# Optimization experiments

Measured on AMD Instinct MI355X. Metric: run time of the kernel, lower is better.

Reference implementation:

```python
import jax, jax.numpy as jnp
import numpy as np

EPS = 1e-9
ROUTING_ITERATIONS = 3


def setup_inputs() -> dict:
    key = jax.random.key(0)
    k1, k2 = jax.random.split(key)
    B, Nin, Din = 32, 2048, 16   # batch, input capsules, input capsule dim
    Nout, Dout = 64, 32          # output capsules, output capsule dim
    x = jax.random.normal(k1, (B, Nin, Din), dtype=jnp.float32)
    # transformation weights W[i, j, d, k] (shared across batch)
    W = jax.random.normal(k2, (Nin, Nout, Dout, Din), dtype=jnp.float32) * 0.05
    bias = jnp.zeros((Nout, Dout), dtype=jnp.float32)
    return {"x": x, "W": W, "bias": bias}


def _squash(s):
    # squash along last axis (capsule vector dim)
    sq_norm = jnp.sum(jnp.square(s), axis=-1, keepdims=True)
    scale = sq_norm / (1.0 + sq_norm)
    return scale * s / jnp.sqrt(sq_norm + EPS)


def reference(x, W, bias):
    # u_hat[b,i,j,d] = sum_k W[i,j,d,k] * x[b,i,k]
    u_hat = jnp.einsum('ijdk,bik->bijd', W, x)
    B, Nin, Nout, Dout = u_hat.shape
    b_log = jnp.zeros((B, Nin, Nout), dtype=u_hat.dtype)  # routing logits
    v = None
    for it in range(ROUTING_ITERATIONS):
        c = jax.nn.softmax(b_log, axis=2)                 # coupling coeffs over Nout
        s = jnp.einsum('bij,bijd->bjd', c, u_hat) + bias  # [B, Nout, Dout]
        v = _squash(s)
        if it < ROUTING_ITERATIONS - 1:
            b_log = b_log + jnp.einsum('bijd,bjd->bij', u_hat, v)
    return v  # [B, Nout, Dout]
```

## Files before the change

kernel.cpp:

```cpp
#include <hip/hip_runtime.h>
#include <hip/hip_bf16.h>
#include <stdint.h>


#define CB    32
#define NIN   2048
#define DIN   16
#define NOUT  64
#define DOUT  32
#define IPB   8
#define NCB   (NIN / IPB)
#define WI    (NOUT * DOUT * DIN)
#define WELEM ((size_t)NIN * WI)

typedef __attribute__((ext_vector_type(8)))  short bf16x8;
typedef __attribute__((ext_vector_type(16))) float f32x16;
typedef _Float16 h2 __attribute__((ext_vector_type(2)));

#define VOFF 0
#define COFF 135168
#define XOFF_IT 143616
#define SMEM_IT  153856
#define SMEM_P0  10240

static __device__ __forceinline__ uint32_t pack_bf2(float a, float b) {
    __hip_bfloat162 hh = __float22bfloat162_rn(make_float2(a, b));
    uint32_t u; __builtin_memcpy(&u, &hh, 4); return u;
}
static __device__ __forceinline__ uint16_t f2bf(float v) {
    return (uint16_t)(pack_bf2(v, 0.f) & 0xffffu);
}
static __device__ __forceinline__ float bf2f(uint16_t u) {
    uint32_t v = (uint32_t)u << 16; float f; __builtin_memcpy(&f, &v, 4); return f;
}
static __device__ __forceinline__ uint32_t pack_h2(float a, float b) {
    h2 r; r.x = (_Float16)a; r.y = (_Float16)b;
    uint32_t u; __builtin_memcpy(&u, &r, 4); return u;
}
static __device__ __forceinline__ h2 as_h2(uint32_t u) {
    h2 r; __builtin_memcpy(&r, &u, 4); return r;
}

__global__ __launch_bounds__(1024, 4) void caps_pass0(
    const float* __restrict__ x, const float* __restrict__ Wf,
    uint32_t* __restrict__ WhOut, uint16_t* __restrict__ s_partial)
{
    extern __shared__ char smem[];
    uint32_t* x_lds = (uint32_t*)smem;

    const int cb = blockIdx.x;
    const int t  = threadIdx.x;
    const int w  = t >> 6, l = t & 63;
    const int bl = l & 31, h = l >> 5;
    const int j0 = w * 4;

    {
        const int b = t >> 5, i = (t >> 2) & 7, k4 = (t & 3) * 4;
        const float4 xv = *(const float4*)(x + ((size_t)b * NIN + cb * IPB + i) * DIN + k4);
        x_lds[(i * 32 + b) * 10 + (k4 >> 1)]     = pack_bf2(xv.x, xv.y);
        x_lds[(i * 32 + b) * 10 + (k4 >> 1) + 1] = pack_bf2(xv.z, xv.w);
    }
    __syncthreads();

    f32x16 sacc[4];
#pragma unroll
    for (int jj = 0; jj < 4; ++jj) sacc[jj] = (f32x16)0.0f;

#pragma unroll 1
    for (int i = 0; i < IPB; ++i) {
        const size_t wbase = (size_t)(cb * IPB + i) * WI;
        bf16x8 bfr;
        {
            uint32_t uu[4];
            const uint32_t* xp = &x_lds[(i * 32 + bl) * 10 + h * 4];
            uu[0] = xp[0]; uu[1] = xp[1]; uu[2] = xp[2]; uu[3] = xp[3];
            __builtin_memcpy(&bfr, uu, 16);
        }
#pragma unroll
        for (int jj = 0; jj < 4; ++jj) {
            const int j = j0 + jj;
            const size_t eoff = wbase + (size_t)(j * 32 + bl) * 16 + h * 8;
            const float4* wp = (const float4*)(Wf + eoff);
            const float4 a4 = wp[0], b4 = wp[1];
            uint32_t uu[4];
            uu[0] = pack_bf2(a4.x, a4.y); uu[1] = pack_bf2(a4.z, a4.w);
            uu[2] = pack_bf2(b4.x, b4.y); uu[3] = pack_bf2(b4.z, b4.w);
            bf16x8 afr; __builtin_memcpy(&afr, uu, 16);
            uint4 st; st.x = uu[0]; st.y = uu[1]; st.z = uu[2]; st.w = uu[3];
            *(uint4*)(WhOut + (eoff >> 1)) = st;
            sacc[jj] = __builtin_amdgcn_mfma_f32_32x32x16_bf16(afr, bfr, sacc[jj], 0, 0, 0);
        }
    }

#pragma unroll
    for (int jj = 0; jj < 4; ++jj) {
        const int j = j0 + jj;
#pragma unroll
        for (int r = 0; r < 16; ++r) {
            const int d = (r & 3) + 8 * (r >> 2) + 4 * h;
            s_partial[(size_t)cb * (2048 * 32) + (size_t)(j * 32 + d) * 32 + bl] =
                f2bf(sacc[jj][r] * (1.0f / 64.0f));
        }
    }
}

template <int IT>
__global__ __launch_bounds__(1024, 4) void caps_it(
    const float* __restrict__ x, const uint16_t* __restrict__ Wh,
    const float* __restrict__ v_prev, const float* __restrict__ blog_in,
    float* __restrict__ blog_out, uint16_t* __restrict__ s_partial)
{
    extern __shared__ char smem[];
    uint32_t* v_lds = (uint32_t*)(smem + VOFF);
    float*    c_lds = (float*)(smem + COFF);
    uint32_t* x_lds = (uint32_t*)(smem + XOFF_IT);

    const int cb = blockIdx.x;
    const int t  = threadIdx.x;
    const int w  = t >> 6, l = t & 63;
    const int bl = l & 31, h = l >> 5;
    const int j0 = w * 4;

    {
        const int b = t >> 5, i = (t >> 2) & 7, k4 = (t & 3) * 4;
        const float4 xv = *(const float4*)(x + ((size_t)b * NIN + cb * IPB + i) * DIN + k4);
        x_lds[(i * 32 + b) * 10 + (k4 >> 1)]     = pack_bf2(xv.x, xv.y);
        x_lds[(i * 32 + b) * 10 + (k4 >> 1) + 1] = pack_bf2(xv.z, xv.w);
    }
#pragma unroll 4
    for (int rep = 0; rep < 32; ++rep) {
        const int idx = rep * 1024 + t;
        const int b = idx >> 10, j = (idx >> 4) & 63, dp = idx & 15;
        const float2 vv = *(const float2*)(v_prev + ((size_t)b * NOUT + j) * DOUT + dp * 2);
        v_lds[(j * 16 + dp) * 33 + b] = pack_h2(vv.x, vv.y);
    }
    __syncthreads();

    f32x16 sacc[4];
#pragma unroll
    for (int jj = 0; jj < 4; ++jj) sacc[jj] = (f32x16)0.0f;

    constexpr int base_dp[8] = {0, 1, 4, 5, 8, 9, 12, 13};

#pragma unroll 1
    for (int i = 0; i < IPB; ++i) {
        const int ig = cb * IPB + i;
        const size_t wbase = (size_t)ig * WI;

        bf16x8 bfr;
        {
            uint32_t uu[4];
            const uint32_t* xp = &x_lds[(i * 32 + bl) * 10 + h * 4];
            uu[0] = xp[0]; uu[1] = xp[1]; uu[2] = xp[2]; uu[3] = xp[3];
            __builtin_memcpy(&bfr, uu, 16);
        }

        uint32_t Dp[4][8];
#pragma unroll
        for (int jj = 0; jj < 4; ++jj) {
            const int j = j0 + jj;
            const bf16x8 afr = *(const bf16x8*)(Wh + wbase + (size_t)(j * 32 + bl) * 16 + h * 8);
            const f32x16 D = __builtin_amdgcn_mfma_f32_32x32x16_bf16(afr, bfr, (f32x16)0.0f, 0, 0, 0);
            float acc = 0.f;
#pragma unroll
            for (int rp = 0; rp < 8; ++rp) {
                const int dp = base_dp[rp] + 2 * h;
                const uint32_t pk = pack_h2(D[2 * rp], D[2 * rp + 1]);
                Dp[jj][rp] = pk;
                acc = __builtin_amdgcn_fdot2(as_h2(pk), as_h2(v_lds[(j * 16 + dp) * 33 + bl]), acc, false);
            }
            acc += __shfl_xor(acc, 32);
            if (h == 0) c_lds[j * 33 + bl] = acc;
        }
        __syncthreads();

#pragma unroll
        for (int rr = 0; rr < 2; ++rr) {
            const int b = w * 2 + rr;
            float bv = c_lds[l * 33 + b];
            if (IT == 2) bv += blog_in[((size_t)b * NIN + ig) * NOUT + l];
            if (IT == 1) blog_out[((size_t)b * NIN + ig) * NOUT + l] = bv;
            float m = bv;
#pragma unroll
            for (int o = 32; o; o >>= 1) m = fmaxf(m, __shfl_xor(m, o));
            const float e = __expf(bv - m);
            float s = e;
#pragma unroll
            for (int o = 32; o; o >>= 1) s += __shfl_xor(s, o);
            c_lds[l * 33 + b] = e / s;
        }
        __syncthreads();

#pragma unroll
        for (int jj = 0; jj < 4; ++jj) {
            const int j = j0 + jj;
            const float cv = c_lds[j * 33 + bl];
#pragma unroll
            for (int rp = 0; rp < 8; ++rp) {
                const h2 hv = as_h2(Dp[jj][rp]);
                sacc[jj][2 * rp]     += cv * (float)hv.x;
                sacc[jj][2 * rp + 1] += cv * (float)hv.y;
            }
        }
        __syncthreads();
    }

#pragma unroll
    for (int jj = 0; jj < 4; ++jj) {
        const int j = j0 + jj;
#pragma unroll
        for (int r = 0; r < 16; ++r) {
            const int d = (r & 3) + 8 * (r >> 2) + 4 * h;
            s_partial[(size_t)cb * (2048 * 32) + (size_t)(j * 32 + d) * 32 + bl] =
                f2bf(sacc[jj][r]);
        }
    }
}

__global__ __launch_bounds__(256) void caps_squash(
    const uint16_t* __restrict__ sp, const float* __restrict__ bias,
    float* __restrict__ vout)
{
    const int j  = blockIdx.x >> 2;
    const int bq = blockIdx.x & 3;
    const int t  = threadIdx.x;
    const int d  = t >> 3;
    const int blq = t & 7;
    const int b  = bq * 8 + blq;

    const uint16_t* p = sp + (size_t)(j * 32 + d) * 32 + b;
    float s0 = 0.f, s1 = 0.f, s2 = 0.f, s3 = 0.f;
#pragma unroll 4
    for (int c = 0; c < NCB; c += 4) {
        s0 += bf2f(p[(size_t)(c + 0) * (2048 * 32)]);
        s1 += bf2f(p[(size_t)(c + 1) * (2048 * 32)]);
        s2 += bf2f(p[(size_t)(c + 2) * (2048 * 32)]);
        s3 += bf2f(p[(size_t)(c + 3) * (2048 * 32)]);
    }
    const float sv = ((s0 + s1) + (s2 + s3)) + bias[j * DOUT + d];

    float sq = sv * sv;
    sq += __shfl_xor(sq, 8);
    sq += __shfl_xor(sq, 16);
    sq += __shfl_xor(sq, 32);

    __shared__ float sh[4][8];
    if ((t & 63) < 8) sh[t >> 6][t & 7] = sq;
    __syncthreads();
    const float tot = sh[0][blq] + sh[1][blq] + sh[2][blq] + sh[3][blq];
    const float scale = (tot / (1.0f + tot)) * rsqrtf(tot + 1e-9f);
    vout[(size_t)b * (NOUT * DOUT) + j * DOUT + d] = scale * sv;
}

extern "C" void kernel_launch(void* const* d_in, const int* in_sizes, int n_in,
                              void* d_out, int out_size, void* d_ws, size_t ws_size,
                              hipStream_t stream) {
    const float* x    = (const float*)d_in[0];
    const float* W    = (const float*)d_in[1];
    const float* bias = (const float*)d_in[2];
    float* out = (float*)d_out;

    char* base = (char*)d_ws;
    uint32_t* Wh    = (uint32_t*)base;
    float*    blog  = (float*)(base + WELEM * 2);
    uint16_t* spart = (uint16_t*)(base + WELEM * 2 + (size_t)CB * NIN * NOUT * 4);
    float*    vbuf  = (float*)(base + WELEM * 2 + (size_t)CB * NIN * NOUT * 4
                               + (size_t)NCB * 2048 * 32 * 2);
    (void)ws_size;

    hipFuncSetAttribute(reinterpret_cast<const void*>(caps_pass0),
                        hipFuncAttributeMaxDynamicSharedMemorySize, SMEM_P0);
    hipFuncSetAttribute(reinterpret_cast<const void*>(caps_it<1>),
                        hipFuncAttributeMaxDynamicSharedMemorySize, SMEM_IT);
    hipFuncSetAttribute(reinterpret_cast<const void*>(caps_it<2>),
                        hipFuncAttributeMaxDynamicSharedMemorySize, SMEM_IT);

    caps_pass0<<<NCB, 1024, SMEM_P0, stream>>>(x, W, (uint32_t*)Wh, spart);
    caps_squash<<<NOUT * 4, 256, 0, stream>>>(spart, bias, vbuf);

    caps_it<1><<<NCB, 1024, SMEM_IT, stream>>>(x, (const uint16_t*)Wh, vbuf, nullptr, blog, spart);
    caps_squash<<<NOUT * 4, 256, 0, stream>>>(spart, bias, vbuf);

    caps_it<2><<<NCB, 1024, SMEM_IT, stream>>>(x, (const uint16_t*)Wh, vbuf, blog, nullptr, spart);
    caps_squash<<<NOUT * 4, 256, 0, stream>>>(spart, bias, out);
}
```

Measured before the change: 273.3 us.

## Fuse all routing passes into one cooperative kernel with grid syncs

```diff
diff --git a/kernel.cpp b/kernel.cpp
--- a/kernel.cpp
+++ b/kernel.cpp
@@ -1,6 +1,9 @@
 #include <hip/hip_runtime.h>
+#include <hip/hip_cooperative_groups.h>
 #include <hip/hip_bf16.h>
 #include <stdint.h>
+
+namespace cg = cooperative_groups;
 
 
 #define CB    32
@@ -17,11 +20,11 @@
 typedef __attribute__((ext_vector_type(16))) float f32x16;
 typedef _Float16 h2 __attribute__((ext_vector_type(2)));
 
-#define VOFF 0
-#define COFF 135168
-#define XOFF_IT 143616
-#define SMEM_IT  153856
-#define SMEM_P0  10240
+#define VOFF    0
+#define COFF    135168
+#define CSTRIDE 2112
+#define XOFF    152064
+#define SMEM_FUSED 162304
 
 static __device__ __forceinline__ uint32_t pack_bf2(float a, float b) {
     __hip_bfloat162 hh = __float22bfloat162_rn(make_float2(a, b));
@@ -41,26 +44,33 @@
     h2 r; __builtin_memcpy(&r, &u, 4); return r;
 }
 
-__global__ __launch_bounds__(1024, 4) void caps_pass0(
-    const float* __restrict__ x, const float* __restrict__ Wf,
-    uint32_t* __restrict__ WhOut, uint16_t* __restrict__ s_partial)
-{
-    extern __shared__ char smem[];
-    uint32_t* x_lds = (uint32_t*)smem;
-
-    const int cb = blockIdx.x;
-    const int t  = threadIdx.x;
-    const int w  = t >> 6, l = t & 63;
+
+static __device__ __forceinline__ void stage_x(const float* __restrict__ x,
+                                               uint32_t* x_lds, int cb, int t) {
+    const int b = t >> 5, i = (t >> 2) & 7, k4 = (t & 3) * 4;
+    const float4 xv = *(const float4*)(x + ((size_t)b * NIN + cb * IPB + i) * DIN + k4);
+    x_lds[(i * 32 + b) * 10 + (k4 >> 1)]     = pack_bf2(xv.x, xv.y);
+    x_lds[(i * 32 + b) * 10 + (k4 >> 1) + 1] = pack_bf2(xv.z, xv.w);
+}
+
+static __device__ __forceinline__ void stage_v(const float* __restrict__ v_prev,
+                                               uint32_t* v_lds, int t) {
+#pragma unroll 4
+    for (int rep = 0; rep < 32; ++rep) {
+        const int idx = rep * 1024 + t;
+        const int b = idx >> 10, j = (idx >> 4) & 63, dp = idx & 15;
+        const float2 vv = *(const float2*)(v_prev + ((size_t)b * NOUT + j) * DOUT + dp * 2);
+        v_lds[(j * 16 + dp) * 33 + b] = pack_h2(vv.x, vv.y);
+    }
+}
+
+static __device__ __forceinline__ void pass0_body(
+    const float* __restrict__ Wf, uint32_t* __restrict__ WhOut,
+    uint16_t* __restrict__ s_partial, const uint32_t* x_lds, int cb, int t)
+{
+    const int w = t >> 6, l = t & 63;
     const int bl = l & 31, h = l >> 5;
     const int j0 = w * 4;
-
-    {
-        const int b = t >> 5, i = (t >> 2) & 7, k4 = (t & 3) * 4;
-        const float4 xv = *(const float4*)(x + ((size_t)b * NIN + cb * IPB + i) * DIN + k4);
-        x_lds[(i * 32 + b) * 10 + (k4 >> 1)]     = pack_bf2(xv.x, xv.y);
-        x_lds[(i * 32 + b) * 10 + (k4 >> 1) + 1] = pack_bf2(xv.z, xv.w);
-    }
-    __syncthreads();
 
     f32x16 sacc[4];
 #pragma unroll
@@ -105,37 +115,15 @@
 }
 
 template <int IT>
-__global__ __launch_bounds__(1024, 4) void caps_it(
-    const float* __restrict__ x, const uint16_t* __restrict__ Wh,
-    const float* __restrict__ v_prev, const float* __restrict__ blog_in,
-    float* __restrict__ blog_out, uint16_t* __restrict__ s_partial)
-{
-    extern __shared__ char smem[];
-    uint32_t* v_lds = (uint32_t*)(smem + VOFF);
-    float*    c_lds = (float*)(smem + COFF);
-    uint32_t* x_lds = (uint32_t*)(smem + XOFF_IT);
-
-    const int cb = blockIdx.x;
-    const int t  = threadIdx.x;
-    const int w  = t >> 6, l = t & 63;
+static __device__ __forceinline__ void it_body(
+    const uint16_t* __restrict__ Wh, const float* __restrict__ blog_in,
+    float* __restrict__ blog_out, uint16_t* __restrict__ s_partial,
+    const uint32_t* v_lds, float* c_lds, const uint32_t* x_lds, int cb, int t)
+{
+    const int w = t >> 6, l = t & 63;
     const int bl = l & 31, h = l >> 5;
     const int j0 = w * 4;
 
-    {
-        const int b = t >> 5, i = (t >> 2) & 7, k4 = (t & 3) * 4;
-        const float4 xv = *(const float4*)(x + ((size_t)b * NIN + cb * IPB + i) * DIN + k4);
-        x_lds[(i * 32 + b) * 10 + (k4 >> 1)]     = pack_bf2(xv.x, xv.y);
-        x_lds[(i * 32 + b) * 10 + (k4 >> 1) + 1] = pack_bf2(xv.z, xv.w);
-    }
-#pragma unroll 4
-    for (int rep = 0; rep < 32; ++rep) {
-        const int idx = rep * 1024 + t;
-        const int b = idx >> 10, j = (idx >> 4) & 63, dp = idx & 15;
-        const float2 vv = *(const float2*)(v_prev + ((size_t)b * NOUT + j) * DOUT + dp * 2);
-        v_lds[(j * 16 + dp) * 33 + b] = pack_h2(vv.x, vv.y);
-    }
-    __syncthreads();
-
     f32x16 sacc[4];
 #pragma unroll
     for (int jj = 0; jj < 4; ++jj) sacc[jj] = (f32x16)0.0f;
@@ -144,6 +132,7 @@
 
 #pragma unroll 1
     for (int i = 0; i < IPB; ++i) {
+        float* cp = c_lds + (i & 1) * CSTRIDE;
         const int ig = cb * IPB + i;
         const size_t wbase = (size_t)ig * WI;
 
@@ -155,7 +144,6 @@
             __builtin_memcpy(&bfr, uu, 16);
         }
 
-        uint32_t Dp[4][8];
 #pragma unroll
         for (int jj = 0; jj < 4; ++jj) {
             const int j = j0 + jj;
@@ -165,19 +153,18 @@
 #pragma unroll
             for (int rp = 0; rp < 8; ++rp) {
                 const int dp = base_dp[rp] + 2 * h;
-                const uint32_t pk = pack_h2(D[2 * rp], D[2 * rp + 1]);
-                Dp[jj][rp] = pk;
-                acc = __builtin_amdgcn_fdot2(as_h2(pk), as_h2(v_lds[(j * 16 + dp) * 33 + bl]), acc, false);
+                h2 dpk; dpk.x = (_Float16)D[2 * rp]; dpk.y = (_Float16)D[2 * rp + 1];
+                acc = __builtin_amdgcn_fdot2(dpk, as_h2(v_lds[(j * 16 + dp) * 33 + bl]), acc, false);
             }
             acc += __shfl_xor(acc, 32);
-            if (h == 0) c_lds[j * 33 + bl] = acc;
+            if (h == 0) cp[j * 33 + bl] = acc;
         }
         __syncthreads();
 
 #pragma unroll
         for (int rr = 0; rr < 2; ++rr) {
             const int b = w * 2 + rr;
-            float bv = c_lds[l * 33 + b];
+            float bv = cp[l * 33 + b];
             if (IT == 2) bv += blog_in[((size_t)b * NIN + ig) * NOUT + l];
             if (IT == 1) blog_out[((size_t)b * NIN + ig) * NOUT + l] = bv;
             float m = bv;
@@ -187,22 +174,18 @@
             float s = e;
 #pragma unroll
             for (int o = 32; o; o >>= 1) s += __shfl_xor(s, o);
-            c_lds[l * 33 + b] = e / s;
+            cp[l * 33 + b] = e / s;
         }
         __syncthreads();
 
 #pragma unroll
         for (int jj = 0; jj < 4; ++jj) {
             const int j = j0 + jj;
-            const float cv = c_lds[j * 33 + bl];
-#pragma unroll
-            for (int rp = 0; rp < 8; ++rp) {
-                const h2 hv = as_h2(Dp[jj][rp]);
-                sacc[jj][2 * rp]     += cv * (float)hv.x;
-                sacc[jj][2 * rp + 1] += cv * (float)hv.y;
-            }
-        }
-        __syncthreads();
+            const bf16x8 afr = *(const bf16x8*)(Wh + wbase + (size_t)(j * 32 + bl) * 16 + h * 8);
+            const f32x16 D = __builtin_amdgcn_mfma_f32_32x32x16_bf16(afr, bfr, (f32x16)0.0f, 0, 0, 0);
+            const float cv = cp[j * 33 + bl];
+            sacc[jj] += D * cv;
+        }
     }
 
 #pragma unroll
@@ -217,46 +200,126 @@
     }
 }
 
-__global__ __launch_bounds__(256) void caps_squash(
+static __device__ __forceinline__ void squash_body(
+    const uint16_t* __restrict__ sp, const float* __restrict__ bias,
+    float* __restrict__ vout, char* smem, int cbid, int t)
+{
+    const int j  = cbid >> 2;
+    const int bq = cbid & 3;
+    const int d   = (t >> 3) & 31;
+    const int blq = t & 7;
+    const int b   = bq * 8 + blq;
+    float sv = 0.f, sq = 0.f;
+    if (t < 256) {
+        const uint16_t* p = sp + (size_t)(j * 32 + d) * 32 + b;
+        float s0 = 0.f, s1 = 0.f, s2 = 0.f, s3 = 0.f;
+#pragma unroll 4
+        for (int c = 0; c < NCB; c += 4) {
+            s0 += bf2f(p[(size_t)(c + 0) * (2048 * 32)]);
+            s1 += bf2f(p[(size_t)(c + 1) * (2048 * 32)]);
+            s2 += bf2f(p[(size_t)(c + 2) * (2048 * 32)]);
+            s3 += bf2f(p[(size_t)(c + 3) * (2048 * 32)]);
+        }
+        sv = ((s0 + s1) + (s2 + s3)) + bias[j * DOUT + d];
+        sq = sv * sv;
+        sq += __shfl_xor(sq, 8);
+        sq += __shfl_xor(sq, 16);
+        sq += __shfl_xor(sq, 32);
+    }
+    float* sh = (float*)smem;
+    if (t < 256 && (t & 63) < 8) sh[(t >> 6) * 8 + (t & 7)] = sq;
+    __syncthreads();
+    if (t < 256) {
+        const float tot = sh[0 * 8 + blq] + sh[1 * 8 + blq] + sh[2 * 8 + blq] + sh[3 * 8 + blq];
+        const float scale = (tot / (1.0f + tot)) * rsqrtf(tot + 1e-9f);
+        vout[(size_t)b * (NOUT * DOUT) + j * DOUT + d] = scale * sv;
+    }
+}
+
+__global__ __launch_bounds__(1024, 4) void caps_fused(
+    const float* __restrict__ x, const float* __restrict__ Wf,
+    uint32_t* __restrict__ Wh, float* __restrict__ blog,
+    uint16_t* __restrict__ spart, const float* __restrict__ bias,
+    float* __restrict__ vbuf, float* __restrict__ out)
+{
+    cg::grid_group grid = cg::this_grid();
+    extern __shared__ char smem[];
+    uint32_t* v_lds = (uint32_t*)(smem + VOFF);
+    float*    c_lds = (float*)(smem + COFF);
+    uint32_t* x_lds = (uint32_t*)(smem + XOFF);
+    const int cb = blockIdx.x;
+    const int t  = threadIdx.x;
+
+    stage_x(x, x_lds, cb, t);
+    __syncthreads();
+
+    pass0_body(Wf, Wh, spart, x_lds, cb, t);
+    __threadfence();
+    grid.sync();
+
+    squash_body(spart, bias, vbuf, smem, cb, t);
+    __threadfence();
+    grid.sync();
+
+    stage_v(vbuf, v_lds, t);
+    __syncthreads();
+    it_body<1>((const uint16_t*)Wh, nullptr, blog, spart, v_lds, c_lds, x_lds, cb, t);
+    __threadfence();
+    grid.sync();
+
+    squash_body(spart, bias, vbuf, smem, cb, t);
+    __threadfence();
+    grid.sync();
+
+    stage_v(vbuf, v_lds, t);
+    __syncthreads();
+    it_body<2>((const uint16_t*)Wh, blog, nullptr, spart, v_lds, c_lds, x_lds, cb, t);
+    __threadfence();
+    grid.sync();
+
+    squash_body(spart, bias, out, smem, cb, t);
+}
+
+__global__ __launch_bounds__(1024, 4) void k_pass0(
+    const float* __restrict__ x, const float* __restrict__ Wf,
+    uint32_t* __restrict__ Wh, uint16_t* __restrict__ spart)
+{
+    extern __shared__ char smem[];
+    uint32_t* x_lds = (uint32_t*)(smem + XOFF);
+    stage_x(x, x_lds, blockIdx.x, threadIdx.x);
+    __syncthreads();
+    pass0_body(Wf, Wh, spart, x_lds, blockIdx.x, threadIdx.x);
+}
+
+template <int IT>
+__global__ __launch_bounds__(1024, 4) void k_it(
+    const float* __restrict__ x, const uint16_t* __restrict__ Wh,
+    const float* __restrict__ v_prev, const float* __restrict__ blog_in,
+    float* __restrict__ blog_out, uint16_t* __restrict__ spart)
+{
+    extern __shared__ char smem[];
+    uint32_t* v_lds = (uint32_t*)(smem + VOFF);
+    float*    c_lds = (float*)(smem + COFF);
+    uint32_t* x_lds = (uint32_t*)(smem + XOFF);
+    stage_x(x, x_lds, blockIdx.x, threadIdx.x);
+    stage_v(v_prev, v_lds, threadIdx.x);
+    __syncthreads();
+    it_body<IT>(Wh, blog_in, blog_out, spart, v_lds, c_lds, x_lds, blockIdx.x, threadIdx.x);
+}
+
+__global__ __launch_bounds__(256) void k_squash(
     const uint16_t* __restrict__ sp, const float* __restrict__ bias,
     float* __restrict__ vout)
 {
-    const int j  = blockIdx.x >> 2;
-    const int bq = blockIdx.x & 3;
-    const int t  = threadIdx.x;
-    const int d  = t >> 3;
-    const int blq = t & 7;
-    const int b  = bq * 8 + blq;
-
-    const uint16_t* p = sp + (size_t)(j * 32 + d) * 32 + b;
-    float s0 = 0.f, s1 = 0.f, s2 = 0.f, s3 = 0.f;
-#pragma unroll 4
-    for (int c = 0; c < NCB; c += 4) {
-        s0 += bf2f(p[(size_t)(c + 0) * (2048 * 32)]);
-        s1 += bf2f(p[(size_t)(c + 1) * (2048 * 32)]);
-        s2 += bf2f(p[(size_t)(c + 2) * (2048 * 32)]);
-        s3 += bf2f(p[(size_t)(c + 3) * (2048 * 32)]);
-    }
-    const float sv = ((s0 + s1) + (s2 + s3)) + bias[j * DOUT + d];
-
-    float sq = sv * sv;
-    sq += __shfl_xor(sq, 8);
-    sq += __shfl_xor(sq, 16);
-    sq += __shfl_xor(sq, 32);
-
-    __shared__ float sh[4][8];
-    if ((t & 63) < 8) sh[t >> 6][t & 7] = sq;
-    __syncthreads();
-    const float tot = sh[0][blq] + sh[1][blq] + sh[2][blq] + sh[3][blq];
-    const float scale = (tot / (1.0f + tot)) * rsqrtf(tot + 1e-9f);
-    vout[(size_t)b * (NOUT * DOUT) + j * DOUT + d] = scale * sv;
+    __shared__ char smem[128];
+    squash_body(sp, bias, vout, smem, blockIdx.x, threadIdx.x);
 }
 
 extern "C" void kernel_launch(void* const* d_in, const int* in_sizes, int n_in,
                               void* d_out, int out_size, void* d_ws, size_t ws_size,
                               hipStream_t stream) {
     const float* x    = (const float*)d_in[0];
-    const float* W    = (const float*)d_in[1];
+    const float* Wf   = (const float*)d_in[1];
     const float* bias = (const float*)d_in[2];
     float* out = (float*)d_out;
 
@@ -268,19 +331,33 @@
                                + (size_t)NCB * 2048 * 32 * 2);
     (void)ws_size;
 
-    hipFuncSetAttribute(reinterpret_cast<const void*>(caps_pass0),
-                        hipFuncAttributeMaxDynamicSharedMemorySize, SMEM_P0);
-    hipFuncSetAttribute(reinterpret_cast<const void*>(caps_it<1>),
-                        hipFuncAttributeMaxDynamicSharedMemorySize, SMEM_IT);
-    hipFuncSetAttribute(reinterpret_cast<const void*>(caps_it<2>),
-                        hipFuncAttributeMaxDynamicSharedMemorySize, SMEM_IT);
-
-    caps_pass0<<<NCB, 1024, SMEM_P0, stream>>>(x, W, (uint32_t*)Wh, spart);
-    caps_squash<<<NOUT * 4, 256, 0, stream>>>(spart, bias, vbuf);
-
-    caps_it<1><<<NCB, 1024, SMEM_IT, stream>>>(x, (const uint16_t*)Wh, vbuf, nullptr, blog, spart);
-    caps_squash<<<NOUT * 4, 256, 0, stream>>>(spart, bias, vbuf);
-
-    caps_it<2><<<NCB, 1024, SMEM_IT, stream>>>(x, (const uint16_t*)Wh, vbuf, blog, nullptr, spart);
-    caps_squash<<<NOUT * 4, 256, 0, stream>>>(spart, bias, out);
-}
+    hipFuncSetAttribute(reinterpret_cast<const void*>(caps_fused),
+                        hipFuncAttributeMaxDynamicSharedMemorySize, SMEM_FUSED);
+    hipFuncSetAttribute(reinterpret_cast<const void*>(k_pass0),
+                        hipFuncAttributeMaxDynamicSharedMemorySize, SMEM_FUSED);
+    hipFuncSetAttribute(reinterpret_cast<const void*>(k_it<1>),
+                        hipFuncAttributeMaxDynamicSharedMemorySize, SMEM_FUSED);
+    hipFuncSetAttribute(reinterpret_cast<const void*>(k_it<2>),
+                        hipFuncAttributeMaxDynamicSharedMemorySize, SMEM_FUSED);
+
+    int dev = 0; hipGetDevice(&dev);
+    int coop = 0;
+    hipDeviceGetAttribute(&coop, hipDeviceAttributeCooperativeLaunch, dev);
+    int nb = 0;
+    hipError_t occ = hipOccupancyMaxActiveBlocksPerMultiprocessor(
+        &nb, reinterpret_cast<const void*>(caps_fused), 1024, SMEM_FUSED);
+
+    if (coop && occ == hipSuccess && nb >= 1) {
+        void* args[] = {(void*)&x, (void*)&Wf, (void*)&Wh, (void*)&blog,
+                        (void*)&spart, (void*)&bias, (void*)&vbuf, (void*)&out};
+        hipLaunchCooperativeKernel(reinterpret_cast<const void*>(caps_fused),
+                                   dim3(NCB), dim3(1024), args, SMEM_FUSED, stream);
+    } else {
+        k_pass0<<<NCB, 1024, SMEM_FUSED, stream>>>(x, Wf, Wh, spart);
+        k_squash<<<NOUT * 4, 256, 0, stream>>>(spart, bias, vbuf);
+        k_it<1><<<NCB, 1024, SMEM_FUSED, stream>>>(x, (const uint16_t*)Wh, vbuf, nullptr, blog, spart);
+        k_squash<<<NOUT * 4, 256, 0, stream>>>(spart, bias, vbuf);
+        k_it<2><<<NCB, 1024, SMEM_FUSED, stream>>>(x, (const uint16_t*)Wh, vbuf, blog, nullptr, spart);
+        k_squash<<<NOUT * 4, 256, 0, stream>>>(spart, bias, out);
+    }
+}
```

New measurement: 252.6 us. -7.6%, faster.

## Split pass0 blocks over output halves and recompute MFMA instead of caching u_hat

Applied to the files above, without the earlier changes.

```diff
diff --git a/kernel.cpp b/kernel.cpp
--- a/kernel.cpp
+++ b/kernel.cpp
@@ -21,7 +21,6 @@
 #define COFF 135168
 #define XOFF_IT 143616
 #define SMEM_IT  153856
-#define SMEM_P0  10240
 
 static __device__ __forceinline__ uint32_t pack_bf2(float a, float b) {
     __hip_bfloat162 hh = __float22bfloat162_rn(make_float2(a, b));
@@ -41,21 +40,23 @@
     h2 r; __builtin_memcpy(&r, &u, 4); return r;
 }
 
-__global__ __launch_bounds__(1024, 4) void caps_pass0(
+__global__ __launch_bounds__(512, 2) void caps_pass0(
     const float* __restrict__ x, const float* __restrict__ Wf,
     uint32_t* __restrict__ WhOut, uint16_t* __restrict__ s_partial)
 {
-    extern __shared__ char smem[];
-    uint32_t* x_lds = (uint32_t*)smem;
-
-    const int cb = blockIdx.x;
+    __shared__ uint32_t x_lds[IPB * 32 * 10];
+
+    const int p  = blockIdx.x;
+    const int cb = p >> 1, jh = p & 1;
     const int t  = threadIdx.x;
     const int w  = t >> 6, l = t & 63;
     const int bl = l & 31, h = l >> 5;
-    const int j0 = w * 4;
-
-    {
-        const int b = t >> 5, i = (t >> 2) & 7, k4 = (t & 3) * 4;
+    const int j0 = jh * 32 + w * 4;
+
+#pragma unroll
+    for (int rep = 0; rep < 2; ++rep) {
+        const int q = t + rep * 512;
+        const int b = q >> 5, i = (q >> 2) & 7, k4 = (q & 3) * 4;
         const float4 xv = *(const float4*)(x + ((size_t)b * NIN + cb * IPB + i) * DIN + k4);
         x_lds[(i * 32 + b) * 10 + (k4 >> 1)]     = pack_bf2(xv.x, xv.y);
         x_lds[(i * 32 + b) * 10 + (k4 >> 1) + 1] = pack_bf2(xv.z, xv.w);
@@ -106,7 +107,7 @@
 
 template <int IT>
 __global__ __launch_bounds__(1024, 4) void caps_it(
-    const float* __restrict__ x, const uint16_t* __restrict__ Wh,
+    const float* __restrict__ x, const uint16_t* __restrict__ Wb,
     const float* __restrict__ v_prev, const float* __restrict__ blog_in,
     float* __restrict__ blog_out, uint16_t* __restrict__ s_partial)
 {
@@ -155,19 +156,17 @@
             __builtin_memcpy(&bfr, uu, 16);
         }
 
-        uint32_t Dp[4][8];
 #pragma unroll
         for (int jj = 0; jj < 4; ++jj) {
             const int j = j0 + jj;
-            const bf16x8 afr = *(const bf16x8*)(Wh + wbase + (size_t)(j * 32 + bl) * 16 + h * 8);
+            const bf16x8 afr = *(const bf16x8*)(Wb + wbase + (size_t)(j * 32 + bl) * 16 + h * 8);
             const f32x16 D = __builtin_amdgcn_mfma_f32_32x32x16_bf16(afr, bfr, (f32x16)0.0f, 0, 0, 0);
             float acc = 0.f;
 #pragma unroll
             for (int rp = 0; rp < 8; ++rp) {
                 const int dp = base_dp[rp] + 2 * h;
-                const uint32_t pk = pack_h2(D[2 * rp], D[2 * rp + 1]);
-                Dp[jj][rp] = pk;
-                acc = __builtin_amdgcn_fdot2(as_h2(pk), as_h2(v_lds[(j * 16 + dp) * 33 + bl]), acc, false);
+                h2 dpk; dpk.x = (_Float16)D[2 * rp]; dpk.y = (_Float16)D[2 * rp + 1];
+                acc = __builtin_amdgcn_fdot2(dpk, as_h2(v_lds[(j * 16 + dp) * 33 + bl]), acc, false);
             }
             acc += __shfl_xor(acc, 32);
             if (h == 0) c_lds[j * 33 + bl] = acc;
@@ -194,13 +193,10 @@
 #pragma unroll
         for (int jj = 0; jj < 4; ++jj) {
             const int j = j0 + jj;
+            const bf16x8 afr = *(const bf16x8*)(Wb + wbase + (size_t)(j * 32 + bl) * 16 + h * 8);
+            const f32x16 D = __builtin_amdgcn_mfma_f32_32x32x16_bf16(afr, bfr, (f32x16)0.0f, 0, 0, 0);
             const float cv = c_lds[j * 33 + bl];
-#pragma unroll
-            for (int rp = 0; rp < 8; ++rp) {
-                const h2 hv = as_h2(Dp[jj][rp]);
-                sacc[jj][2 * rp]     += cv * (float)hv.x;
-                sacc[jj][2 * rp + 1] += cv * (float)hv.y;
-            }
+            sacc[jj] += D * cv;
         }
         __syncthreads();
     }
@@ -268,14 +264,12 @@
                                + (size_t)NCB * 2048 * 32 * 2);
     (void)ws_size;
 
-    hipFuncSetAttribute(reinterpret_cast<const void*>(caps_pass0),
-                        hipFuncAttributeMaxDynamicSharedMemorySize, SMEM_P0);
     hipFuncSetAttribute(reinterpret_cast<const void*>(caps_it<1>),
                         hipFuncAttributeMaxDynamicSharedMemorySize, SMEM_IT);
     hipFuncSetAttribute(reinterpret_cast<const void*>(caps_it<2>),
                         hipFuncAttributeMaxDynamicSharedMemorySize, SMEM_IT);
 
-    caps_pass0<<<NCB, 1024, SMEM_P0, stream>>>(x, W, (uint32_t*)Wh, spart);
+    caps_pass0<<<NCB * 2, 512, 0, stream>>>(x, W, Wh, spart);
     caps_squash<<<NOUT * 4, 256, 0, stream>>>(spart, bias, vbuf);
 
     caps_it<1><<<NCB, 1024, SMEM_IT, stream>>>(x, (const uint16_t*)Wh, vbuf, nullptr, blog, spart);
```

New measurement: 246.9 us. 9.7% less time.
